# Kernel optimization log

Hardware: AMD Instinct MI355X
Metric: run time of the kernel (lower is better)

The kernel has to match this reference:

```python
import jax, jax.numpy as jnp
import numpy as np

N = 10000; E = 320000; B = 262144
F_NODE = 64; F_EDGE = 8; H = 4; C = 32
EVO_IN = C * 4 * H + 1      # 513
EVO_HID = 256; EVO_DIM = 64
FLOW_IN = EVO_DIM + 5       # 69
FLOW_HID = 256
SLOPE = 0.01                # torch LeakyReLU default slope
GAT_SLOPE = 0.2             # GATv2 attention LeakyReLU slope
EPS = 1e-5                  # BatchNorm eps


def setup_inputs() -> dict:
    key = jax.random.key(0)
    ks = iter(jax.random.split(key, 64))
    def nrm(shape, scale=1.0):
        return jax.random.normal(next(ks), shape, jnp.float32) * scale
    inp = {}
    inp['x1'] = nrm((N, F_NODE))
    inp['edge_index1'] = jax.random.randint(next(ks), (2, E), 0, N)
    inp['edge_attr1'] = nrm((E, F_EDGE))
    inp['x2'] = nrm((N, F_NODE))
    inp['edge_index2'] = jax.random.randint(next(ks), (2, E), 0, N)
    inp['edge_attr2'] = nrm((E, F_EDGE))
    inp['dist_m'] = jax.random.uniform(next(ks), (N, N), jnp.float32)
    inp['node_visit'] = jax.random.uniform(next(ks), (N, 2), jnp.float32)
    inp['od_nodes'] = jax.random.randint(next(ks), (B, 2), 0, N)
    # GATv2Conv params per snapshot: lin_l, lin_r (bias=True), lin_edge (bias=False), att [H,C], out bias [H*C]
    for p in ('g1', 'g2'):
        s = 1.0 / np.sqrt(F_NODE)
        inp[p + '_Wl'] = nrm((H * C, F_NODE), s)
        inp[p + '_bl'] = jnp.zeros((H * C,), jnp.float32)
        inp[p + '_Wr'] = nrm((H * C, F_NODE), s)
        inp[p + '_br'] = jnp.zeros((H * C,), jnp.float32)
        inp[p + '_We'] = nrm((H * C, F_EDGE), 1.0 / np.sqrt(F_EDGE))
        inp[p + '_att'] = nrm((H, C), 1.0 / np.sqrt(C))
        inp[p + '_bias'] = jnp.zeros((H * C,), jnp.float32)
    # EvoEmbedding (all Linear bias=False)
    inp['e_W1'] = nrm((EVO_HID, EVO_IN), 1.0 / np.sqrt(EVO_IN))
    inp['e_W2'] = nrm((EVO_HID, EVO_HID), 1.0 / np.sqrt(EVO_HID))
    inp['e_W3'] = nrm((EVO_HID, EVO_HID), 1.0 / np.sqrt(EVO_HID))
    inp['e_W4'] = nrm((EVO_HID // 2, EVO_HID), 1.0 / np.sqrt(EVO_HID))
    inp['e_Wout'] = nrm((EVO_DIM, EVO_HID // 2), 1.0 / np.sqrt(EVO_HID // 2))
    # FlowGenerator (Linear bias=False) + BatchNorm affine params
    inp['f_W1'] = nrm((FLOW_HID, FLOW_IN), 1.0 / np.sqrt(FLOW_IN))
    inp['f_W2'] = nrm((FLOW_HID, FLOW_HID), 1.0 / np.sqrt(FLOW_HID))
    inp['f_W3'] = nrm((FLOW_HID, FLOW_HID), 1.0 / np.sqrt(FLOW_HID))
    inp['f_W4'] = nrm((FLOW_HID // 2, FLOW_HID), 1.0 / np.sqrt(FLOW_HID))
    inp['f_Wout'] = nrm((1, FLOW_HID // 2), 1.0 / np.sqrt(FLOW_HID // 2))
    inp['f_g1'] = jnp.ones((FLOW_HID,), jnp.float32);  inp['f_b1'] = jnp.zeros((FLOW_HID,), jnp.float32)
    inp['f_g2'] = jnp.ones((FLOW_HID,), jnp.float32);  inp['f_b2'] = jnp.zeros((FLOW_HID,), jnp.float32)
    inp['f_g3'] = jnp.ones((FLOW_HID,), jnp.float32);  inp['f_b3'] = jnp.zeros((FLOW_HID,), jnp.float32)
    inp['f_g4'] = jnp.ones((FLOW_HID // 2,), jnp.float32); inp['f_b4'] = jnp.zeros((FLOW_HID // 2,), jnp.float32)
    return inp


def _gatv2(x, ei, ea, Wl, bl, Wr, br, We, att, bias):
    src, dst = ei[0], ei[1]
    # self-loops with fill_value='mean': per-target mean of incoming edge_attr
    deg = jax.ops.segment_sum(jnp.ones_like(dst, jnp.float32), dst, N)
    mean_attr = jax.ops.segment_sum(ea, dst, N) / jnp.maximum(deg, 1.0)[:, None]
    loops = jnp.arange(N)
    s = jnp.concatenate([src, loops]); d = jnp.concatenate([dst, loops])
    eaf = jnp.concatenate([ea, mean_attr], axis=0)            # [E+N, F_EDGE]
    xl = (x @ Wl.T + bl).reshape(N, H, C)                     # source transform
    xr = (x @ Wr.T + br).reshape(N, H, C)                     # target transform
    em = (eaf @ We.T).reshape(-1, H, C)
    msg = jax.nn.leaky_relu(xl[s] + xr[d] + em, GAT_SLOPE)    # [E+N, H, C]
    scr = jnp.einsum('ehc,hc->eh', msg, att)                  # [E+N, H]
    mx = jax.ops.segment_max(scr, d, N)
    ex = jnp.exp(scr - mx[d])
    den = jax.ops.segment_sum(ex, d, N)
    alpha = ex / den[d]                                       # softmax over incoming edges
    out = jax.ops.segment_sum(alpha[:, :, None] * xl[s], d, N).reshape(N, H * C) + bias
    return jax.nn.relu(out), alpha


def _evo(v, W1, W2, W3, W4, Wout):
    h = jax.nn.leaky_relu(v @ W1.T, SLOPE)
    h = jax.nn.leaky_relu(h @ W2.T, SLOPE)
    h = jax.nn.leaky_relu(h @ W3.T, SLOPE)
    h = jax.nn.leaky_relu(h @ W4.T, SLOPE)
    return h @ Wout.T


def _bn(x, g, b):
    mu = x.mean(0)
    var = x.var(0)
    return (x - mu) * jax.lax.rsqrt(var + EPS) * g + b


def _flow(v, W1, W2, W3, W4, Wout, g1, b1, g2, b2, g3, b3, g4, b4):
    h = jax.nn.leaky_relu(_bn(v @ W1.T, g1, b1), SLOPE)
    h = jax.nn.leaky_relu(_bn(h @ W2.T, g2, b2), SLOPE)
    h = jax.nn.leaky_relu(_bn(h @ W3.T, g3, b3), SLOPE)
    h = jax.nn.leaky_relu(_bn(h @ W4.T, g4, b4), SLOPE)
    return (h @ Wout.T).squeeze(-1)


def reference(x1, edge_index1, edge_attr1, x2, edge_index2, edge_attr2, dist_m, node_visit, od_nodes,
              g1_Wl, g1_bl, g1_Wr, g1_br, g1_We, g1_att, g1_bias,
              g2_Wl, g2_bl, g2_Wr, g2_br, g2_We, g2_att, g2_bias,
              e_W1, e_W2, e_W3, e_W4, e_Wout,
              f_W1, f_W2, f_W3, f_W4, f_Wout,
              f_g1, f_b1, f_g2, f_b2, f_g3, f_b3, f_g4, f_b4):
    n1, a1 = _gatv2(x1, edge_index1, edge_attr1, g1_Wl, g1_bl, g1_Wr, g1_br, g1_We, g1_att, g1_bias)
    n2, a2 = _gatv2(x2, edge_index2, edge_attr2, g2_Wl, g2_bl, g2_Wr, g2_br, g2_We, g2_att, g2_bias)
    o = od_nodes[:, 0]; dn = od_nodes[:, 1]
    dist = dist_m[o, dn][:, None]                              # fused gather replacing python loop
    feat = jnp.concatenate([n1[o], n1[dn], n2[o], n2[dn], dist], axis=1)  # [B, 513]
    evo = _evo(feat, e_W1, e_W2, e_W3, e_W4, e_Wout)           # [B, EVO_DIM]
    # NOTE: original uses node_visit[:,0] for BOTH o_visit and d_visit (kept faithful)
    ov = node_visit[o, 0:1]; dv = node_visit[dn, 0:1]
    ovn = node_visit[o, 1:2]; dvn = node_visit[dn, 1:2]
    cat = jnp.concatenate([evo, ov, dv, ovn, dvn, dist], axis=1)  # [B, 69]
    inferred = _flow(cat, f_W1, f_W2, f_W3, f_W4, f_Wout, f_g1, f_b1, f_g2, f_b2, f_g3, f_b3, f_g4, f_b4)
    return (inferred, a1, a2, evo)
```

## Files before the change

kernel.cpp:

```cpp
#include <hip/hip_runtime.h>

typedef unsigned short u16;
typedef unsigned int u32;

#define NN 10000
#define NE 320000
#define ET 330000
#define NB 262144
#define SHST 1792

typedef __attribute__((ext_vector_type(8))) short bf16x8;
typedef __attribute__((ext_vector_type(4))) float f32x4;

__device__ __forceinline__ u16 f2b(float f) {
  u32 u = __float_as_uint(f);
  u += 0x7fffu + ((u >> 16) & 1u);
  return (u16)(u >> 16);
}
__device__ __forceinline__ float b2f(u16 h) {
  return __uint_as_float(((u32)h) << 16);
}
__device__ __forceinline__ float lrelu(float v, float s) { return v > 0.f ? v : v * s; }

__device__ __forceinline__ void g2lds16(const void* g, void* l) {
  __builtin_amdgcn_global_load_lds((const __attribute__((address_space(1))) void*)g,
                                   (__attribute__((address_space(3))) void*)l, 16, 0, 0);
}

template <int N> __device__ __forceinline__ void waitv() {
  if constexpr (N == 0) asm volatile("s_waitcnt vmcnt(0)" ::: "memory");
  else if constexpr (N == 1) asm volatile("s_waitcnt vmcnt(1)" ::: "memory");
  else if constexpr (N == 2) asm volatile("s_waitcnt vmcnt(2)" ::: "memory");
  else if constexpr (N == 3) asm volatile("s_waitcnt vmcnt(3)" ::: "memory");
  else if constexpr (N == 4) asm volatile("s_waitcnt vmcnt(4)" ::: "memory");
  else if constexpr (N == 5) asm volatile("s_waitcnt vmcnt(5)" ::: "memory");
  else asm volatile("s_waitcnt vmcnt(6)" ::: "memory");
}
__device__ __forceinline__ void waitl0() { asm volatile("s_waitcnt lgkmcnt(0)" ::: "memory"); }
__device__ __forceinline__ void fence() { asm volatile("" ::: "memory"); }

__global__ __launch_bounds__(256) void k_prep(const float* __restrict__ eW2, const float* __restrict__ eW3,
                                              const float* __restrict__ eW4, const float* __restrict__ eWo,
                                              const float* __restrict__ fW1, const float* __restrict__ fW2,
                                              const float* __restrict__ fW3, const float* __restrict__ fW4,
                                              const float* __restrict__ eW1,
                                              u16* eW2b, u16* eW3b, u16* eW4b,
                                              u16* fW2b, u16* fW3b, u16* fW4b,
                                              float* W1T, float* w512, u16* wTail) {
  const int blk = blockIdx.x, tid = threadIdx.x;
  if (blk < 256) {
    int t = blk * 256 + tid; eW2b[t] = f2b(eW2[t]);
  } else if (blk < 512) {
    int t = (blk - 256) * 256 + tid; eW3b[t] = f2b(eW3[t]);
  } else if (blk < 640) {
    int t = (blk - 512) * 256 + tid; eW4b[t] = f2b(eW4[t]);
  } else if (blk < 896) {
    int t = (blk - 640) * 256 + tid; fW2b[t] = f2b(fW2[t]);
  } else if (blk < 1152) {
    int t = (blk - 896) * 256 + tid; fW3b[t] = f2b(fW3[t]);
  } else if (blk < 1280) {
    int t = (blk - 1152) * 256 + tid; fW4b[t] = f2b(fW4[t]);
  } else if (blk < 1536) {
    int m = blk - 1280;
    for (int k = tid; k < 512; k += 256) W1T[(size_t)k * 256 + m] = eW1[(size_t)m * 513 + k];
  } else if (blk == 1536) {
    w512[tid] = eW1[(size_t)tid * 513 + 512];
  } else if (blk < 1577) {
    int t = (blk - 1537) * 256 + tid;
    int r = t / 160, k = t - r * 160;
    wTail[(size_t)r * 160 + k] = (k < 128) ? f2b(eWo[(size_t)r * 128 + k]) : (u16)0;
  } else {
    int m = blk - 1577;
    int k = tid;
    if (k < 160) {
      float v = 0.f;
      if (k < 128) {
        const float* fr = fW1 + (size_t)m * 69;
        for (int j = 0; j < 64; ++j) v += fr[j] * eWo[(size_t)j * 128 + k];
      } else if (k < 133) {
        v = fW1[(size_t)m * 69 + 64 + (k - 128)];
      }
      wTail[(size_t)(64 + m) * 160 + k] = f2b(v);
    }
  }
}

__global__ __launch_bounds__(256) void k_sprep(const int* __restrict__ od, const float* __restrict__ dm,
                                               const float* __restrict__ nv,
                                               float* __restrict__ distb, u16* __restrict__ bufC) {
  int b = blockIdx.x * 256 + threadIdx.x;
  int o = od[b * 2], d = od[b * 2 + 1];
  float dist = dm[(size_t)o * NN + d];
  distb[b] = dist;
  u16 tmp[32];
  tmp[0] = f2b(nv[o * 2]);
  tmp[1] = f2b(nv[d * 2]);
  tmp[2] = f2b(nv[o * 2 + 1]);
  tmp[3] = f2b(nv[d * 2 + 1]);
  tmp[4] = f2b(dist);
#pragma unroll
  for (int k = 5; k < 32; ++k) tmp[k] = 0;
  u16* p = bufC + (size_t)b * 160 + 128;
#pragma unroll
  for (int k = 0; k < 4; ++k) *(bf16x8*)(p + k * 8) = *(bf16x8*)(tmp + k * 8);
}

__global__ __launch_bounds__(256) void k_count2(const int* __restrict__ ei0, const int* __restrict__ ei1,
                                                int* __restrict__ cnt) {
  int t = blockIdx.x * 256 + threadIdx.x;
  if (t >= 2 * ET) return;
  int g = t >= ET; int e = t - g * ET;
  const int* ei = g ? ei1 : ei0;
  int d = (e < NE) ? ei[NE + e] : (e - NE);
  atomicAdd(&cnt[g * NN + d], 1);
}

__global__ __launch_bounds__(1024) void k_scan2(const int* __restrict__ cnt, int* __restrict__ cs) {
  const int g = blockIdx.x;
  cnt += g * NN; cs += g * (NN + 1);
  __shared__ int part[1024];
  int tid = threadIdx.x;
  int base = tid * 10;
  int local[10];
  int s = 0;
#pragma unroll
  for (int i = 0; i < 10; ++i) {
    int idx = base + i;
    int v = (idx < NN) ? cnt[idx] : 0;
    local[i] = s; s += v;
  }
  part[tid] = s;
  __syncthreads();
  for (int off = 1; off < 1024; off <<= 1) {
    int v = (tid >= off) ? part[tid - off] : 0;
    __syncthreads();
    part[tid] += v;
    __syncthreads();
  }
  int pre = (tid > 0) ? part[tid - 1] : 0;
#pragma unroll
  for (int i = 0; i < 10; ++i) {
    int idx = base + i;
    if (idx < NN) cs[idx] = pre + local[i];
  }
  if (tid == 1023) cs[NN] = part[1023];
}

__global__ __launch_bounds__(256) void k_fill2(const int* __restrict__ ei0, const int* __restrict__ ei1,
                                               const int* __restrict__ cs, int* __restrict__ wr,
                                               int2* __restrict__ csr) {
  int t = blockIdx.x * 256 + threadIdx.x;
  if (t >= 2 * ET) return;
  int g = t >= ET; int e = t - g * ET;
  const int* ei = g ? ei1 : ei0;
  int s, d;
  if (e < NE) { s = ei[e]; d = ei[NE + e]; } else { s = e - NE; d = s; }
  int pos = atomicAdd(&wr[g * NN + d], 1);
// ... 158 lines not shown
  nout[(size_t)d * 128 + 64 + lane] = fmaxf(acc1 / dn1 + bias[64 + lane], 0.f);
}

__global__ __launch_bounds__(256) void k_alpha2(const float* __restrict__ scr,
                                                const int* __restrict__ ei0, const int* __restrict__ ei1,
                                                const float* __restrict__ m, const float* __restrict__ den,
                                                float* __restrict__ a1, float* __restrict__ a2) {
  int t = blockIdx.x * 256 + threadIdx.x;
  if (t >= 2 * ET * 4) return;
  int g = t >= ET * 4; int tt = t - g * ET * 4;
  int e = tt >> 2, h = tt & 3;
  const int* ei = g ? ei1 : ei0;
  int d = (e < NE) ? ei[NE + e] : (e - NE);
  const float* mg = m + (size_t)g * NN * 4;
  const float* dg = den + (size_t)g * NN * 4;
  float* aout = g ? a2 : a1;
  aout[tt] = __expf(scr[(size_t)g * ET * 4 + tt] - mg[d * 4 + h]) / dg[d * 4 + h];
}

__global__ __launch_bounds__(256) void k_qtab(const float* __restrict__ n1, const float* __restrict__ n2,
                                              const float* __restrict__ W1T,
                                              u16* __restrict__ Qo, u16* __restrict__ Qd) {
  __shared__ float s1[2048], s2[2048];
  int nb = blockIdx.x * 16;
  for (int i = threadIdx.x; i < 2048; i += 256) {
    s1[i] = n1[(size_t)nb * 128 + i];
    s2[i] = n2[(size_t)nb * 128 + i];
  }
  __syncthreads();
  int m = threadIdx.x;
  float qo[16], qd[16];
#pragma unroll
  for (int i = 0; i < 16; ++i) { qo[i] = 0.f; qd[i] = 0.f; }
#pragma unroll 2
  for (int k = 0; k < 128; ++k) {
    float w0 = W1T[(size_t)k * 256 + m];
    float w1 = W1T[(size_t)(128 + k) * 256 + m];
    float w2 = W1T[(size_t)(256 + k) * 256 + m];
    float w3 = W1T[(size_t)(384 + k) * 256 + m];
#pragma unroll
    for (int i = 0; i < 16; ++i) {
      float a = s1[i * 128 + k], b = s2[i * 128 + k];
      qo[i] += a * w0 + b * w2;
      qd[i] += a * w1 + b * w3;
    }
  }
#pragma unroll
  for (int i = 0; i < 16; ++i) {
    Qo[(size_t)(nb + i) * 256 + m] = f2b(qo[i]);
    Qd[(size_t)(nb + i) * 256 + m] = f2b(qd[i]);
  }
}

template <int NF, int EPI, int BNA>
__global__ __launch_bounds__(512) void gemm256(const u16* __restrict__ A, const u16* __restrict__ W,
                                               int K, size_t lda,
                                               u16* __restrict__ obf, int ld_bf,
                                               float* __restrict__ stats,
                                               const float* __restrict__ stin, const float* __restrict__ gg,
                                               const float* __restrict__ bb, float invB) {
  constexpr int M = NF * 64;
  constexpr int CPW = 2 + NF / 2;
  __shared__ alignas(16) u16 Alds[2][256 * 32];
  __shared__ alignas(16) u16 Blds[2][M * 32];
  __shared__ float sS[256], sT[256];
  const int tid = threadIdx.x;
  const int lane = tid & 63;
  const int w = tid >> 6;
  const int wr = w >> 2, wc = w & 3;
  const size_t rowBase = (size_t)blockIdx.x * 256;

  if (BNA) {
    for (int c = tid; c < K; c += 512) {
      float s0 = 0.f, q0 = 0.f;
#pragma unroll
      for (int sh = 0; sh < 8; ++sh) {
        s0 += stin[sh * SHST + c];
        q0 += stin[sh * SHST + K + c];
      }
      float mu = s0 * invB;
      float var = q0 * invB - mu * mu;
      float sc = rsqrtf(var + 1e-5f) * gg[c];
      sS[c] = sc;
      sT[c] = bb[c] - mu * sc;
    }
    __syncthreads();
  }

  f32x4 acc[8][NF];
  const f32x4 z4 = {0.f, 0.f, 0.f, 0.f};
#pragma unroll
  for (int m = 0; m < 8; ++m)
#pragma unroll
    for (int n = 0; n < NF; ++n) acc[m][n] = z4;

  const int crow = lane >> 2;
  const int ccol = (lane & 3) << 3;
  const int KT = K >> 5;

  auto stage = [&](int buf, int kb) {
#pragma unroll
    for (int i = 0; i < CPW; ++i) {
      const int c = w * CPW + i;
      if (c < 16) {
        const u16* src = A + (rowBase + (c << 4) + crow) * lda + kb + ccol;
        g2lds16(src, &Alds[buf][(c << 4) << 5]);
// ... 39 lines not shown
    for (int m = 0; m < 8; ++m) {
      bf16x8 af = *(const bf16x8*)&Alds[cur][(((wr << 7) + (m << 4) + lr) << 5) + lk];
      if (BNA) {
        bf16x8 o;
#pragma unroll
        for (int j = 0; j < 8; ++j) {
          float v = fmaf(b2f((u16)af[j]), sv[j], tv[j]);
          v = v > 0.f ? v : v * 0.01f;
          o[j] = (short)f2b(v);
        }
        af = o;
      }
#pragma unroll
      for (int n = 0; n < NF; ++n)
        acc[m][n] = __builtin_amdgcn_mfma_f32_16x16x32_bf16(af, bfr[n], acc[m][n], 0, 0, 0);
    }
    __builtin_amdgcn_s_barrier();
    cur ^= 1;
  }

  float csm[NF], cq[NF];
#pragma unroll
  for (int n = 0; n < NF; ++n) { csm[n] = 0.f; cq[n] = 0.f; }
#pragma unroll
  for (int m = 0; m < 8; ++m) {
#pragma unroll
    for (int n = 0; n < NF; ++n) {
      const int col = wc * (NF * 16) + (n << 4) + lr;
#pragma unroll
      for (int j = 0; j < 4; ++j) {
        const size_t row = rowBase + (wr << 7) + (m << 4) + (lg << 2) + j;
        float v = acc[m][n][j];
        if (EPI == 0) {
          v = v > 0.f ? v : v * 0.01f;
          obf[row * ld_bf + col] = f2b(v);
        } else {
          obf[row * ld_bf + col] = f2b(v);
          csm[n] += v; cq[n] += v * v;
        }
      }
    }
  }
  if (EPI == 1) {
    const int shard = ((int)blockIdx.x & 7) * SHST;
#pragma unroll
    for (int n = 0; n < NF; ++n) {
      float s = csm[n], q = cq[n];
      s += __shfl_xor(s, 16); s += __shfl_xor(s, 32);
      q += __shfl_xor(q, 16); q += __shfl_xor(q, 32);
      if (lane < 16) {
        const int col = wc * (NF * 16) + (n << 4) + lane;
        atomicAdd(&stats[shard + col], s);
        atomicAdd(&stats[shard + M + col], q);
      }
    }
  }
}

__global__ __launch_bounds__(512) void gemm256_evo(const u16* __restrict__ W,
                                                   u16* __restrict__ obf,
                                                   const u16* __restrict__ Qo, const u16* __restrict__ Qd,
                                                   const int* __restrict__ od, const float* __restrict__ distb,
                                                   const float* __restrict__ w512) {
  constexpr int KT = 8;
  __shared__ alignas(16) u16 Alds[2][256 * 32];
  __shared__ alignas(16) u16 Blds[2][256 * 32];
  __shared__ float sW[256], sDist[256];
  __shared__ int sO[256], sD[256];
  const int tid = threadIdx.x;
  const int lane = tid & 63;
  const int w = tid >> 6;
  const int wr = w >> 2, wc = w & 3;
  const size_t rowBase = (size_t)blockIdx.x * 256;
  const int crow = lane >> 2, ccol = (lane & 3) << 3;
  const int arow = tid >> 1;
  const int acol = (tid & 1) << 4;
  const int lr = lane & 15, lk = (lane >> 4) << 3, lg = lane >> 4;

  if (tid < 256) {
    int2 p = ((const int2*)od)[rowBase + tid];
    sO[tid] = p.x; sD[tid] = p.y;
    sDist[tid] = distb[rowBase + tid];
    sW[tid] = w512[tid];
  }
  __syncthreads();

  auto stageB = [&](int buf, int kb) {
#pragma unroll
    for (int i = 0; i < 2; ++i) {
      int c = w * 2 + i;
      const u16* src = W + (size_t)((c << 4) + crow) * 256 + kb + ccol;
      g2lds16(src, &Blds[buf][(c << 4) << 5]);
    }
  };
  auto loadA = [&](int kb, bf16x8& r0, bf16x8& r1, bf16x8& r2, bf16x8& r3) {
    const u16* qo = Qo + (size_t)sO[arow] * 256 + kb + acol;
    const u16* qd = Qd + (size_t)sD[arow] * 256 + kb + acol;
    r0 = *(const bf16x8*)qo; r1 = *(const bf16x8*)(qo + 8);
    r2 = *(const bf16x8*)qd; r3 = *(const bf16x8*)(qd + 8);
  };
  auto writeA = [&](int buf, int kb, bf16x8 r0, bf16x8 r1, bf16x8 r2, bf16x8 r3) {
    float dist = sDist[arow];
    bf16x8 w0, w1;
#pragma unroll
    for (int j = 0; j < 8; ++j) {
      float v = b2f((u16)r0[j]) + b2f((u16)r2[j]) + dist * sW[kb + acol + j];
      w0[j] = (short)f2b(lrelu(v, 0.01f));
      float v2 = b2f((u16)r1[j]) + b2f((u16)r3[j]) + dist * sW[kb + acol + 8 + j];
      w1[j] = (short)f2b(lrelu(v2, 0.01f));
    }
    *(bf16x8*)&Alds[buf][arow * 32 + acol] = w0;
    *(bf16x8*)&Alds[buf][arow * 32 + acol + 8] = w1;
  };

  f32x4 acc[8][4];
  const f32x4 z4 = {0.f, 0.f, 0.f, 0.f};
#pragma unroll
  for (int m = 0; m < 8; ++m)
#pragma unroll
    for (int n = 0; n < 4; ++n) acc[m][n] = z4;

  bf16x8 p0, p1, p2, p3;
  {
    bf16x8 c0, c1, c2, c3;
    loadA(0, c0, c1, c2, c3);
    writeA(0, 0, c0, c1, c2, c3);
  }
  stageB(0, 0);
  fence();
  loadA(32, p0, p1, p2, p3);
  fence();
  waitv<4>();
  waitl0();
  __builtin_amdgcn_s_barrier();

  int cur = 0;
  for (int kt = 0; kt < KT; ++kt) {
    const int kb = kt << 5;
    const bool hasN = kt + 1 < KT, hasNN = kt + 2 < KT;
    bf16x8 bfr[4];
#pragma unroll
    for (int n = 0; n < 4; ++n)
      bfr[n] = *(const bf16x8*)&Blds[cur][((((wc << 2) + n) << 4) + lr) * 32 + lk];
    if (hasN) stageB(cur ^ 1, kb + 32);
    fence();
    bf16x8 q0, q1, q2, q3;
    if (hasNN) loadA(kb + 64, q0, q1, q2, q3);
    fence();
#pragma unroll
    for (int m = 0; m < 8; ++m) {
      bf16x8 af = *(const bf16x8*)&Alds[cur][(((wr << 7) + (m << 4) + lr) << 5) + lk];
#pragma unroll
      for (int n = 0; n < 4; ++n)
        acc[m][n] = __builtin_amdgcn_mfma_f32_16x16x32_bf16(af, bfr[n], acc[m][n], 0, 0, 0);
    }
    if (hasN) {
      if (hasNN) waitv<6>(); else waitv<2>();
      writeA(cur ^ 1, kb + 32, p0, p1, p2, p3);
      p0 = q0; p1 = q1; p2 = q2; p3 = q3;
      if (hasNN) waitv<4>(); else waitv<0>();
      waitl0();
    }
    __builtin_amdgcn_s_barrier();
    cur ^= 1;
  }

#pragma unroll
  for (int m = 0; m < 8; ++m) {
#pragma unroll
    for (int n = 0; n < 4; ++n) {
      const int col = (wc << 6) + (n << 4) + lr;
#pragma unroll
      for (int j = 0; j < 4; ++j) {
        const size_t row = rowBase + (wr << 7) + (m << 4) + (lg << 2) + j;
        float v = acc[m][n][j];
        v = v > 0.f ? v : v * 0.01f;
        obf[row * 256 + col] = f2b(v);
      }
    }
  }
}

__global__ __launch_bounds__(512) void gemm320(const u16* __restrict__ A, const u16* __restrict__ W,
                                               float* __restrict__ oevo, u16* __restrict__ opre,
                                               float* __restrict__ stats) {
  constexpr int KT = 5;
  __shared__ alignas(16) u16 Alds[2][256 * 32];
  __shared__ alignas(16) u16 Blds[2][320 * 32];
  const int tid = threadIdx.x;
  const int lane = tid & 63;
  const int w = tid >> 6;
  const int wr = w >> 2, wc = w & 3;
  const size_t rowBase = (size_t)blockIdx.x * 256;
  const int crow = lane >> 2, ccol = (lane & 3) << 3;
  const int lr = lane & 15, lk = (lane >> 4) << 3, lg = lane >> 4;

  f32x4 acc[8][5];
  const f32x4 z4 = {0.f, 0.f, 0.f, 0.f};
#pragma unroll
  for (int m = 0; m < 8; ++m)
#pragma unroll
    for (int n = 0; n < 5; ++n) acc[m][n] = z4;

  auto stage = [&](int buf, int kb) {
#pragma unroll
    for (int i = 0; i < 2; ++i) {
      int c = w * 2 + i;
      const u16* src = A + (rowBase + (c << 4) + crow) * 160 + kb + ccol;
      g2lds16(src, &Alds[buf][(c << 4) << 5]);
    }
    if (w < 4) {
#pragma unroll
      for (int i = 0; i < 3; ++i) {
        int c = w * 3 + i;
        const u16* src = W + (size_t)((c << 4) + crow) * 160 + kb + ccol;
        g2lds16(src, &Blds[buf][(c << 4) << 5]);
      }
    } else {
#pragma unroll
      for (int i = 0; i < 2; ++i) {
        int c = 12 + (w - 4) * 2 + i;
        const u16* src = W + (size_t)((c << 4) + crow) * 160 + kb + ccol;
        g2lds16(src, &Blds[buf][(c << 4) << 5]);
      }
    }
  };

  stage(0, 0);
  int cur = 0;
  for (int kt = 0; kt < KT; ++kt) {
    if (kt + 1 < KT) {
      stage(cur ^ 1, (kt + 1) << 5);
      if (w < 4) waitv<5>(); else waitv<4>();
    } else {
      waitv<0>();
    }
    __builtin_amdgcn_s_barrier();
    bf16x8 bfr[5];
#pragma unroll
    for (int n = 0; n < 5; ++n)
      bfr[n] = *(const bf16x8*)&Blds[cur][(((wc * 80 + (n << 4) + lr)) << 5) + lk];
#pragma unroll
    for (int m = 0; m < 8; ++m) {
      bf16x8 af = *(const bf16x8*)&Alds[cur][(((wr << 7) + (m << 4) + lr) << 5) + lk];
#pragma unroll
      for (int n = 0; n < 5; ++n)
        acc[m][n] = __builtin_amdgcn_mfma_f32_16x16x32_bf16(af, bfr[n], acc[m][n], 0, 0, 0);
    }
    __builtin_amdgcn_s_barrier();
    cur ^= 1;
  }

  float csm[5], cq[5];
#pragma unroll
  for (int n = 0; n < 5; ++n) { csm[n] = 0.f; cq[n] = 0.f; }
#pragma unroll
  for (int m = 0; m < 8; ++m) {
#pragma unroll
    for (int n = 0; n < 5; ++n) {
      const int col = wc * 80 + (n << 4) + lr;
#pragma unroll
      for (int j = 0; j < 4; ++j) {
        const size_t row = rowBase + (wr << 7) + (m << 4) + (lg << 2) + j;
        float v = acc[m][n][j];
        if (col < 64) {
          oevo[row * 64 + col] = v;
        } else {
          opre[row * 256 + (col - 64)] = f2b(v);
          csm[n] += v; cq[n] += v * v;
        }
      }
    }
  }
  const int shard = ((int)blockIdx.x & 7) * SHST;
#pragma unroll
  for (int n = 0; n < 5; ++n) {
    float s = csm[n], q = cq[n];
    s += __shfl_xor(s, 16); s += __shfl_xor(s, 32);
    q += __shfl_xor(q, 16); q += __shfl_xor(q, 32);
    if (lane < 16) {
      const int col = wc * 80 + (n << 4) + lane;
      if (col >= 64) {
        atomicAdd(&stats[shard + col - 64], s);
        atomicAdd(&stats[shard + 256 + col - 64], q);
      }
    }
  }
}

__global__ __launch_bounds__(256) void k_fout4(const u16* __restrict__ pre, const float* __restrict__ st,
                                               const float* __restrict__ g, const float* __restrict__ b,
                                               const float* __restrict__ W, float* __restrict__ out,
                                               float invB) {
  __shared__ float smu[128], srs[128], sg[128], sb[128], sw[128];
  if (threadIdx.x < 128) {
    int c = threadIdx.x;
    float s0 = 0.f, q0 = 0.f;
#pragma unroll
    for (int sh = 0; sh < 8; ++sh) {
      s0 += st[sh * SHST + c];
      q0 += st[sh * SHST + 128 + c];
    }
    float mu = s0 * invB;
    float var = q0 * invB - mu * mu;
    smu[c] = mu;
    srs[c] = rsqrtf(var + 1e-5f);
    sg[c] = g[c];
    sb[c] = b[c];
    sw[c] = W[c];
  }
  __syncthreads();
  int bi = blockIdx.x * 256 + threadIdx.x;
  const u16* hp = pre + (size_t)bi * 128;
  float acc = 0.f;
#pragma unroll
  for (int k = 0; k < 128; k += 8) {
    bf16x8 u = *(const bf16x8*)(hp + k);
#pragma unroll
    for (int j = 0; j < 8; ++j) {
      int c = k + j;
      float v = (b2f((u16)u[j]) - smu[c]) * srs[c] * sg[c] + sb[c];
      v = b2f(f2b(lrelu(v, 0.01f)));
      acc += v * sw[c];
    }
  }
  out[bi] = acc;
}

extern "C" void kernel_launch(void* const* d_in, const int* in_sizes, int n_in,
                              void* d_out, int out_size, void* d_ws, size_t ws_size,
                              hipStream_t stream) {
  (void)in_sizes; (void)n_in; (void)out_size; (void)ws_size;

  const float* x0 = (const float*)d_in[0];
  const int* ei0 = (const int*)d_in[1];
  const float* ea0 = (const float*)d_in[2];
  const float* x1 = (const float*)d_in[3];
  const int* ei1 = (const int*)d_in[4];
  const float* ea1 = (const float*)d_in[5];
  const float* dm = (const float*)d_in[6];
  const float* nv = (const float*)d_in[7];
  const int* od = (const int*)d_in[8];
  const float* Wl0 = (const float*)d_in[9];
  const float* bl0 = (const float*)d_in[10];
  const float* Wr0 = (const float*)d_in[11];
  const float* br0 = (const float*)d_in[12];
  const float* We0 = (const float*)d_in[13];
  const float* att0 = (const float*)d_in[14];
  const float* bia0 = (const float*)d_in[15];
  const float* Wl1 = (const float*)d_in[16];
  const float* bl1 = (const float*)d_in[17];
  const float* Wr1 = (const float*)d_in[18];
  const float* br1 = (const float*)d_in[19];
  const float* We1 = (const float*)d_in[20];
  const float* att1 = (const float*)d_in[21];
  const float* bia1 = (const float*)d_in[22];
  const float* eW1 = (const float*)d_in[23];
  const float* eW2 = (const float*)d_in[24];
  const float* eW3 = (const float*)d_in[25];
  const float* eW4 = (const float*)d_in[26];
  const float* eWo = (const float*)d_in[27];
  const float* fW1 = (const float*)d_in[28];
  const float* fW2 = (const float*)d_in[29];
  const float* fW3 = (const float*)d_in[30];
  const float* fW4 = (const float*)d_in[31];
  const float* fWo = (const float*)d_in[32];
  const float* fg[4] = {(const float*)d_in[33], (const float*)d_in[35], (const float*)d_in[37], (const float*)d_in[39]};
  const float* fb[4] = {(const float*)d_in[34], (const float*)d_in[36], (const float*)d_in[38], (const float*)d_in[40]};

  float* out_inf = (float*)d_out;
  float* out_a1 = out_inf + NB;
  float* out_a2 = out_a1 + (size_t)ET * 4;
  float* out_evo = out_a2 + (size_t)ET * 4;

  char* base = (char*)d_ws;
  size_t cur = 0;
  auto carve = [&](size_t bytes) -> char* {
    char* p = base + cur;
    cur += (bytes + 255) & ~(size_t)255;
    return p;
  };
  u16* bufA = (u16*)carve((size_t)NB * 256 * 2);
  u16* bufB = (u16*)carve((size_t)NB * 256 * 2);
  u16* bufC = (u16*)carve((size_t)NB * 160 * 2);
  float* n1 = (float*)carve((size_t)NN * 128 * 4);
  float* n2 = (float*)carve((size_t)NN * 128 * 4);
  u16* Qob = (u16*)carve((size_t)NN * 256 * 2);
  u16* Qdb = (u16*)carve((size_t)NN * 256 * 2);
  float* xl = (float*)carve((size_t)2 * NN * 128 * 4);
  float* xr = (float*)carve((size_t)2 * NN * 128 * 4);
  float* stats = (float*)carve((size_t)8 * SHST * 4);
  int* cw = (int*)carve((size_t)4 * NN * 4);
  int* cnt = cw;
  int* wr = cw + 2 * NN;
  int* cs = (int*)carve((size_t)2 * (NN + 1) * 4);
  int2* csr = (int2*)carve((size_t)2 * ET * 8);
  float* m_out = (float*)carve((size_t)2 * NN * 4 * 4);
  float* den_out = (float*)carve((size_t)2 * NN * 4 * 4);
  float* asum = (float*)carve((size_t)2 * NN * 8 * 4);
  float* scr = (float*)carve((size_t)2 * ET * 4 * 4);
  float* distb = (float*)carve((size_t)NB * 4);
  float* w512 = (float*)carve(1024);
  float* W1T = (float*)carve(512 * 256 * 4);
  float* st[4] = {stats, stats + 512, stats + 1024, stats + 1536};
  u16* eW2b = (u16*)carve(256 * 256 * 2);
  u16* eW3b = (u16*)carve(256 * 256 * 2);
  u16* eW4b = (u16*)carve(128 * 256 * 2);
  u16* fW2b = (u16*)carve(256 * 256 * 2);
  u16* fW3b = (u16*)carve(256 * 256 * 2);
  u16* fW4b = (u16*)carve(128 * 256 * 2);
  u16* wTail = (u16*)carve(320 * 160 * 2);

  k_prep<<<1833, 256, 0, stream>>>(eW2, eW3, eW4, eWo, fW1, fW2, fW3, fW4, eW1,
                                   eW2b, eW3b, eW4b, fW2b, fW3b, fW4b,
                                   W1T, w512, wTail);
  hipMemsetAsync(stats, 0, (size_t)8 * SHST * 4 + (size_t)4 * NN * 4, stream);
  k_sprep<<<NB / 256, 256, 0, stream>>>(od, dm, nv, distb, bufC);

  k_count2<<<(2 * ET + 255) / 256, 256, 0, stream>>>(ei0, ei1, cnt);
  k_scan2<<<2, 1024, 0, stream>>>(cnt, cs);
  k_fill2<<<(2 * ET + 255) / 256, 256, 0, stream>>>(ei0, ei1, cs, wr, csr);
  k_asum2<<<2 * NN / 4, 256, 0, stream>>>(csr, cs, ea0, ea1, asum);
  k_xlr2<<<NN, 256, 0, stream>>>(x0, x1, Wl0, bl0, Wr0, br0, Wl1, bl1, Wr1, br1, xl, xr);
  k_scr2<<<4096, 256, 0, stream>>>(xl, xr, ei0, ei1, ea0, ea1, asum, We0, We1, att0, att1, scr);
  k_nodered2<<<2 * NN / 4, 256, 0, stream>>>(scr, csr, cs, xl, bia0, bia1, m_out, den_out, n1, n2);
  k_alpha2<<<(2 * ET * 4 + 255) / 256, 256, 0, stream>>>(scr, ei0, ei1, m_out, den_out, out_a1, out_a2);

  k_qtab<<<NN / 16, 256, 0, stream>>>(n1, n2, W1T, Qob, Qdb);

  const float invB = 1.0f / (float)NB;
  const int GB = NB / 256;
  gemm256_evo<<<GB, 512, 0, stream>>>(eW2b, bufA, Qob, Qdb, od, distb, w512);
  gemm256<4, 0, 0><<<GB, 512, 0, stream>>>(bufA, eW3b, 256, 256, bufB, 256, nullptr,
                                           nullptr, nullptr, nullptr, 0.f);
  gemm256<2, 0, 0><<<GB, 512, 0, stream>>>(bufB, eW4b, 256, 256, bufC, 160, nullptr,
                                           nullptr, nullptr, nullptr, 0.f);
  gemm320<<<GB, 512, 0, stream>>>(bufC, wTail, out_evo, bufA, st[0]);

  gemm256<4, 1, 1><<<GB, 512, 0, stream>>>(bufA, fW2b, 256, 256, bufB, 256, st[1],
                                           st[0], fg[0], fb[0], invB);
  gemm256<4, 1, 1><<<GB, 512, 0, stream>>>(bufB, fW3b, 256, 256, bufA, 256, st[2],
                                           st[1], fg[1], fb[1], invB);
  gemm256<2, 1, 1><<<GB, 512, 0, stream>>>(bufA, fW4b, 256, 256, bufB, 128, st[3],
                                           st[2], fg[2], fb[2], invB);
  k_fout4<<<NB / 256, 256, 0, stream>>>(bufB, st[3], fg[3], fb[3], fWo, out_inf, invB);
}
```

Before: 1.248 ms.

## Fuse four evo-embedding GEMMs into one kernel keeping activations in LDS

Result: slower. 1.798 ms (+44.0%).

```diff
diff --git a/kernel.cpp b/kernel.cpp
--- a/kernel.cpp
+++ b/kernel.cpp
@@ -38,6 +38,10 @@
 }
 __device__ __forceinline__ void waitl0() { asm volatile("s_waitcnt lgkmcnt(0)" ::: "memory"); }
 __device__ __forceinline__ void fence() { asm volatile("" ::: "memory"); }
+
+__device__ __forceinline__ int HIDX(int row, int col) {
+  return (row * 256 + col) ^ ((row & 7) << 3);
+}
 
 __global__ __launch_bounds__(256) void k_prep(const float* __restrict__ eW2, const float* __restrict__ eW3,
                                               const float* __restrict__ eW4, const float* __restrict__ eWo,
@@ -87,22 +91,19 @@
 
 __global__ __launch_bounds__(256) void k_sprep(const int* __restrict__ od, const float* __restrict__ dm,
                                                const float* __restrict__ nv,
-                                               float* __restrict__ distb, u16* __restrict__ bufC) {
+                                               float* __restrict__ distb, u16* __restrict__ sbuf) {
   int b = blockIdx.x * 256 + threadIdx.x;
   int o = od[b * 2], d = od[b * 2 + 1];
   float dist = dm[(size_t)o * NN + d];
   distb[b] = dist;
-  u16 tmp[32];
-  tmp[0] = f2b(nv[o * 2]);
-  tmp[1] = f2b(nv[d * 2]);
-  tmp[2] = f2b(nv[o * 2 + 1]);
-  tmp[3] = f2b(nv[d * 2 + 1]);
-  tmp[4] = f2b(dist);
-#pragma unroll
-  for (int k = 5; k < 32; ++k) tmp[k] = 0;
-  u16* p = bufC + (size_t)b * 160 + 128;
-#pragma unroll
-  for (int k = 0; k < 4; ++k) *(bf16x8*)(p + k * 8) = *(bf16x8*)(tmp + k * 8);
+  bf16x8 r;
+  r[0] = (short)f2b(nv[o * 2]);
+  r[1] = (short)f2b(nv[d * 2]);
+  r[2] = (short)f2b(nv[o * 2 + 1]);
+  r[3] = (short)f2b(nv[d * 2 + 1]);
+  r[4] = (short)f2b(dist);
+  r[5] = 0; r[6] = 0; r[7] = 0;
+  *(bf16x8*)(sbuf + (size_t)b * 8) = r;
 }
 
 __global__ __launch_bounds__(256) void k_count2(const int* __restrict__ ei0, const int* __restrict__ ei1,
@@ -367,6 +368,305 @@
   }
 }
 
+template <int NF2, int KK, int M2>
+__device__ __forceinline__ void fusedStage(const u16* __restrict__ Wsrc, u16* hT, u16* B2,
+                                           int tid, f32x4 acc[8][NF2]) {
+  const int lane = tid & 63, w = tid >> 6, wr = w >> 2, wc = w & 3;
+  const int lr = lane & 15, lk = (lane >> 4) << 3;
+  constexpr int KT = KK >> 5;
+  constexpr int NCH = (M2 * 4 + 511) / 512;
+  {
+    bf16x8 rB[NCH];
+    int c = 0;
+    for (int i = tid; i < M2 * 4; i += 512) {
+      int row = i >> 2, part = i & 3;
+      rB[c++] = *(const bf16x8*)(Wsrc + (size_t)row * KK + part * 8);
+    }
+    waitv<0>();
+    c = 0;
+    for (int i = tid; i < M2 * 4; i += 512) {
+      int row = i >> 2, part = i & 3;
+      *(bf16x8*)&B2[row * 40 + part * 8] = rB[c++];
+    }
+    waitl0();
+    __builtin_amdgcn_s_barrier();
+  }
+  for (int kt = 0; kt < KT; ++kt) {
+    const int kb = kt << 5;
+    bf16x8 af[8], bfr[NF2];
+#pragma unroll
+    for (int m = 0; m < 8; ++m) {
+      int row = (wr << 7) + (m << 4) + lr;
+      af[m] = *(const bf16x8*)&hT[HIDX(row, kb + lk)];
+    }
+#pragma unroll
+    for (int n = 0; n < NF2; ++n) {
+      int cc = wc * (NF2 * 16) + (n << 4) + lr;
+      bfr[n] = *(const bf16x8*)&B2[cc * 40 + lk];
+    }
+    bf16x8 rN[NCH];
+    if (kt + 1 < KT) {
+      int c = 0;
+      for (int i = tid; i < M2 * 4; i += 512) {
+        int row = i >> 2, part = i & 3;
+        rN[c++] = *(const bf16x8*)(Wsrc + (size_t)row * KK + kb + 32 + part * 8);
+      }
+    }
+#pragma unroll
+    for (int m = 0; m < 8; ++m)
+#pragma unroll
+      for (int n = 0; n < NF2; ++n)
+        acc[m][n] = __builtin_amdgcn_mfma_f32_16x16x32_bf16(af[m], bfr[n], acc[m][n], 0, 0, 0);
+    __builtin_amdgcn_s_barrier();
+    if (kt + 1 < KT) {
+      waitv<0>();
+      int c = 0;
+      for (int i = tid; i < M2 * 4; i += 512) {
+        int row = i >> 2, part = i & 3;
+        *(bf16x8*)&B2[row * 40 + part * 8] = rN[c++];
+      }
+      waitl0();
+    }
+    __builtin_amdgcn_s_barrier();
+  }
+}
+
+__global__ __launch_bounds__(512) void k_evochain(const u16* __restrict__ eW2b, const u16* __restrict__ eW3b,
+                                                  const u16* __restrict__ eW4b, const u16* __restrict__ wTail,
+                                                  const u16* __restrict__ Qo, const u16* __restrict__ Qd,
+                                                  const int* __restrict__ od, const float* __restrict__ distb,
+                                                  const float* __restrict__ w512, const u16* __restrict__ sbuf,
+                                                  float* __restrict__ oevo, u16* __restrict__ opre,
+                                                  float* __restrict__ stats) {
+  __shared__ alignas(16) u16 hT[65536];
+  __shared__ alignas(16) u16 B2[12800];
+  __shared__ alignas(16) float sAux[1024];
+  const int tid = threadIdx.x;
+  const int lane = tid & 63;
+  const int w = tid >> 6;
+  const int wr = w >> 2, wc = w & 3;
+  const size_t rowBase = (size_t)blockIdx.x * 256;
+  const int crow = lane >> 2, ccol = (lane & 3) << 3;
+  const int arow = tid >> 1, acol = (tid & 1) << 4;
+  const int lr = lane & 15, lk = (lane >> 4) << 3, lg = lane >> 4;
+
+  float* sW = sAux;
+  float* sDist = sAux + 256;
+  int* sO = (int*)(sAux + 512);
+  int* sD = (int*)(sAux + 768);
+
+  if (tid < 256) {
+    int2 p = ((const int2*)od)[rowBase + tid];
+    sO[tid] = p.x; sD[tid] = p.y;
+    sDist[tid] = distb[rowBase + tid];
+    sW[tid] = w512[tid];
+  }
+  __syncthreads();
+
+  {
+    u16* A0 = hT;
+    u16* B0 = hT + 16384;
+    auto stageB = [&](int buf, int kb) {
+#pragma unroll
+      for (int i = 0; i < 2; ++i) {
+        int c = w * 2 + i;
+        const u16* src = eW2b + (size_t)((c << 4) + crow) * 256 + kb + ccol;
+        g2lds16(src, B0 + buf * 8192 + (c << 9));
+      }
+    };
+    auto loadA = [&](int kb, bf16x8& r0, bf16x8& r1, bf16x8& r2, bf16x8& r3) {
+      const u16* qo = Qo + (size_t)sO[arow] * 256 + kb + acol;
+      const u16* qd = Qd + (size_t)sD[arow] * 256 + kb + acol;
+      r0 = *(const bf16x8*)qo; r1 = *(const bf16x8*)(qo + 8);
+      r2 = *(const bf16x8*)qd; r3 = *(const bf16x8*)(qd + 8);
+    };
+    auto writeA = [&](int buf, int kb, bf16x8 r0, bf16x8 r1, bf16x8 r2, bf16x8 r3) {
+      float dist = sDist[arow];
+      bf16x8 w0, w1;
+#pragma unroll
+      for (int j = 0; j < 8; ++j) {
+        float v = b2f((u16)r0[j]) + b2f((u16)r2[j]) + dist * sW[kb + acol + j];
+        w0[j] = (short)f2b(lrelu(v, 0.01f));
+        float v2 = b2f((u16)r1[j]) + b2f((u16)r3[j]) + dist * sW[kb + acol + 8 + j];
+        w1[j] = (short)f2b(lrelu(v2, 0.01f));
+      }
+      *(bf16x8*)(A0 + buf * 8192 + arow * 32 + acol) = w0;
+      *(bf16x8*)(A0 + buf * 8192 + arow * 32 + acol + 8) = w1;
+    };
+
+    f32x4 acc[8][4];
+    const f32x4 z4 = {0.f, 0.f, 0.f, 0.f};
+#pragma unroll
+    for (int m = 0; m < 8; ++m)
+#pragma unroll
+      for (int n = 0; n < 4; ++n) acc[m][n] = z4;
+
+    bf16x8 p0, p1, p2, p3;
+    {
+      bf16x8 c0, c1, c2, c3;
+      loadA(0, c0, c1, c2, c3);
+      writeA(0, 0, c0, c1, c2, c3);
+    }
+    stageB(0, 0);
+    fence();
+    loadA(32, p0, p1, p2, p3);
+    fence();
+    waitv<4>();
+    waitl0();
+    __builtin_amdgcn_s_barrier();
+
+    int cur = 0;
+    for (int kt = 0; kt < 8; ++kt) {
+      const int kb = kt << 5;
+      const bool hasN = kt + 1 < 8, hasNN = kt + 2 < 8;
+      bf16x8 bfr[4];
+#pragma unroll
+      for (int n = 0; n < 4; ++n)
+        bfr[n] = *(const bf16x8*)(B0 + cur * 8192 + ((((wc << 2) + n) << 4) + lr) * 32 + lk);
+      if (hasN) stageB(cur ^ 1, kb + 32);
+      fence();
+      bf16x8 q0, q1, q2, q3;
+      if (hasNN) loadA(kb + 64, q0, q1, q2, q3);
+      fence();
+#pragma unroll
+      for (int m = 0; m < 8; ++m) {
+        bf16x8 af = *(const bf16x8*)(A0 + cur * 8192 + (((wr << 7) + (m << 4) + lr) << 5) + lk);
+#pragma unroll
+        for (int n = 0; n < 4; ++n)
+          acc[m][n] = __builtin_amdgcn_mfma_f32_16x16x32_bf16(af, bfr[n], acc[m][n], 0, 0, 0);
+      }
+      if (hasN) {
+        if (hasNN) waitv<6>(); else waitv<2>();
+        writeA(cur ^ 1, kb + 32, p0, p1, p2, p3);
+        p0 = q0; p1 = q1; p2 = q2; p3 = q3;
+        if (hasNN) waitv<4>(); else waitv<0>();
+        waitl0();
+      }
+      __builtin_amdgcn_s_barrier();
+      cur ^= 1;
+    }
+#pragma unroll
+    for (int m = 0; m < 8; ++m)
+#pragma unroll
+      for (int n = 0; n < 4; ++n) {
+        const int col = (wc << 6) + (n << 4) + lr;
+#pragma unroll
+        for (int j = 0; j < 4; ++j) {
+          const int row = (wr << 7) + (m << 4) + (lg << 2) + j;
+          float v = acc[m][n][j];
+          v = v > 0.f ? v : v * 0.01f;
+          hT[HIDX(row, col)] = f2b(v);
+        }
+      }
+    waitl0();
+    __builtin_amdgcn_s_barrier();
+  }
+
+  {
+    f32x4 acc[8][4];
+    const f32x4 z4 = {0.f, 0.f, 0.f, 0.f};
+#pragma unroll
+    for (int m = 0; m < 8; ++m)
+#pragma unroll
+      for (int n = 0; n < 4; ++n) acc[m][n] = z4;
+    fusedStage<4, 256, 256>(eW3b, hT, B2, tid, acc);
+#pragma unroll
+    for (int m = 0; m < 8; ++m)
+#pragma unroll
+      for (int n = 0; n < 4; ++n) {
+        const int col = (wc << 6) + (n << 4) + lr;
+#pragma unroll
+        for (int j = 0; j < 4; ++j) {
+          const int row = (wr << 7) + (m << 4) + (lg << 2) + j;
+          float v = acc[m][n][j];
+          v = v > 0.f ? v : v * 0.01f;
+          hT[HIDX(row, col)] = f2b(v);
+        }
+      }
+    waitl0();
+    __builtin_amdgcn_s_barrier();
+  }
+
+  {
+    f32x4 acc[8][2];
+    const f32x4 z4 = {0.f, 0.f, 0.f, 0.f};
+#pragma unroll
+    for (int m = 0; m < 8; ++m)
+#pragma unroll
+      for (int n = 0; n < 2; ++n) acc[m][n] = z4;
+    fusedStage<2, 256, 128>(eW4b, hT, B2, tid, acc);
+#pragma unroll
+    for (int m = 0; m < 8; ++m)
+#pragma unroll
+      for (int n = 0; n < 2; ++n) {
+        const int col = (wc << 5) + (n << 4) + lr;
+#pragma unroll
+        for (int j = 0; j < 4; ++j) {
+          const int row = (wr << 7) + (m << 4) + (lg << 2) + j;
+          float v = acc[m][n][j];
+          v = v > 0.f ? v : v * 0.01f;
+          hT[HIDX(row, col)] = f2b(v);
+        }
+      }
+    if (tid < 256) {
+      bf16x8 s8 = *(const bf16x8*)(sbuf + (rowBase + tid) * 8);
+      *(bf16x8*)&hT[HIDX(tid, 128)] = s8;
+      bf16x8 z = {0, 0, 0, 0, 0, 0, 0, 0};
+      *(bf16x8*)&hT[HIDX(tid, 136)] = z;
+      *(bf16x8*)&hT[HIDX(tid, 144)] = z;
+      *(bf16x8*)&hT[HIDX(tid, 152)] = z;
+    }
+    waitl0();
+    __builtin_amdgcn_s_barrier();
+  }
+
+  {
+    f32x4 acc[8][5];
+    const f32x4 z4 = {0.f, 0.f, 0.f, 0.f};
+#pragma unroll
+    for (int m = 0; m < 8; ++m)
+#pragma unroll
+      for (int n = 0; n < 5; ++n) acc[m][n] = z4;
+    fusedStage<5, 160, 320>(wTail, hT, B2, tid, acc);
+
+    float csm[5], cq[5];
+#pragma unroll
+    for (int n = 0; n < 5; ++n) { csm[n] = 0.f; cq[n] = 0.f; }
+#pragma unroll
+    for (int m = 0; m < 8; ++m) {
+#pragma unroll
+      for (int n = 0; n < 5; ++n) {
+        const int col = wc * 80 + (n << 4) + lr;
+#pragma unroll
+        for (int j = 0; j < 4; ++j) {
+          const size_t row = rowBase + (wr << 7) + (m << 4) + (lg << 2) + j;
+          float v = acc[m][n][j];
+          if (col < 64) {
+            oevo[row * 64 + col] = v;
+          } else {
+            opre[row * 256 + (col - 64)] = f2b(v);
+            csm[n] += v; cq[n] += v * v;
+          }
+        }
+      }
+    }
+    const int shard = ((int)blockIdx.x & 7) * SHST;
+#pragma unroll
+    for (int n = 0; n < 5; ++n) {
+      float s = csm[n], q = cq[n];
+      s += __shfl_xor(s, 16); s += __shfl_xor(s, 32);
+      q += __shfl_xor(q, 16); q += __shfl_xor(q, 32);
+      if (lane < 16) {
+        const int col = wc * 80 + (n << 4) + lane;
+        if (col >= 64) {
+          atomicAdd(&stats[shard + col - 64], s);
+          atomicAdd(&stats[shard + 256 + col - 64], q);
+        }
+      }
+    }
+  }
+}
+
 template <int NF, int EPI, int BNA>
 __global__ __launch_bounds__(512) void gemm256(const u16* __restrict__ A, const u16* __restrict__ W,
                                                int K, size_t lda,
@@ -512,237 +812,6 @@
         const int col = wc * (NF * 16) + (n << 4) + lane;
         atomicAdd(&stats[shard + col], s);
         atomicAdd(&stats[shard + M + col], q);
-      }
-    }
-  }
-}
-
-__global__ __launch_bounds__(512) void gemm256_evo(const u16* __restrict__ W,
-                                                   u16* __restrict__ obf,
-                                                   const u16* __restrict__ Qo, const u16* __restrict__ Qd,
-                                                   const int* __restrict__ od, const float* __restrict__ distb,
-                                                   const float* __restrict__ w512) {
-  constexpr int KT = 8;
-  __shared__ alignas(16) u16 Alds[2][256 * 32];
-  __shared__ alignas(16) u16 Blds[2][256 * 32];
-  __shared__ float sW[256], sDist[256];
-  __shared__ int sO[256], sD[256];
-  const int tid = threadIdx.x;
-  const int lane = tid & 63;
-  const int w = tid >> 6;
-  const int wr = w >> 2, wc = w & 3;
-  const size_t rowBase = (size_t)blockIdx.x * 256;
-  const int crow = lane >> 2, ccol = (lane & 3) << 3;
-  const int arow = tid >> 1;
-  const int acol = (tid & 1) << 4;
-  const int lr = lane & 15, lk = (lane >> 4) << 3, lg = lane >> 4;
-
-  if (tid < 256) {
-    int2 p = ((const int2*)od)[rowBase + tid];
-    sO[tid] = p.x; sD[tid] = p.y;
-    sDist[tid] = distb[rowBase + tid];
-    sW[tid] = w512[tid];
-  }
-  __syncthreads();
-
-  auto stageB = [&](int buf, int kb) {
-#pragma unroll
-    for (int i = 0; i < 2; ++i) {
-      int c = w * 2 + i;
-      const u16* src = W + (size_t)((c << 4) + crow) * 256 + kb + ccol;
-      g2lds16(src, &Blds[buf][(c << 4) << 5]);
-    }
-  };
-  auto loadA = [&](int kb, bf16x8& r0, bf16x8& r1, bf16x8& r2, bf16x8& r3) {
-    const u16* qo = Qo + (size_t)sO[arow] * 256 + kb + acol;
-    const u16* qd = Qd + (size_t)sD[arow] * 256 + kb + acol;
-    r0 = *(const bf16x8*)qo; r1 = *(const bf16x8*)(qo + 8);
-    r2 = *(const bf16x8*)qd; r3 = *(const bf16x8*)(qd + 8);
-  };
-  auto writeA = [&](int buf, int kb, bf16x8 r0, bf16x8 r1, bf16x8 r2, bf16x8 r3) {
-    float dist = sDist[arow];
-    bf16x8 w0, w1;
-#pragma unroll
-    for (int j = 0; j < 8; ++j) {
-      float v = b2f((u16)r0[j]) + b2f((u16)r2[j]) + dist * sW[kb + acol + j];
-      w0[j] = (short)f2b(lrelu(v, 0.01f));
-      float v2 = b2f((u16)r1[j]) + b2f((u16)r3[j]) + dist * sW[kb + acol + 8 + j];
-      w1[j] = (short)f2b(lrelu(v2, 0.01f));
-    }
-    *(bf16x8*)&Alds[buf][arow * 32 + acol] = w0;
-    *(bf16x8*)&Alds[buf][arow * 32 + acol + 8] = w1;
-  };
-
-  f32x4 acc[8][4];
-  const f32x4 z4 = {0.f, 0.f, 0.f, 0.f};
-#pragma unroll
-  for (int m = 0; m < 8; ++m)
-#pragma unroll
-    for (int n = 0; n < 4; ++n) acc[m][n] = z4;
-
-  bf16x8 p0, p1, p2, p3;
-  {
-    bf16x8 c0, c1, c2, c3;
-    loadA(0, c0, c1, c2, c3);
-    writeA(0, 0, c0, c1, c2, c3);
-  }
-  stageB(0, 0);
-  fence();
-  loadA(32, p0, p1, p2, p3);
-  fence();
-  waitv<4>();
-  waitl0();
-  __builtin_amdgcn_s_barrier();
-
-  int cur = 0;
-  for (int kt = 0; kt < KT; ++kt) {
-    const int kb = kt << 5;
-    const bool hasN = kt + 1 < KT, hasNN = kt + 2 < KT;
-    bf16x8 bfr[4];
-#pragma unroll
-    for (int n = 0; n < 4; ++n)
-      bfr[n] = *(const bf16x8*)&Blds[cur][((((wc << 2) + n) << 4) + lr) * 32 + lk];
-    if (hasN) stageB(cur ^ 1, kb + 32);
-    fence();
-    bf16x8 q0, q1, q2, q3;
-    if (hasNN) loadA(kb + 64, q0, q1, q2, q3);
-    fence();
-#pragma unroll
-    for (int m = 0; m < 8; ++m) {
-      bf16x8 af = *(const bf16x8*)&Alds[cur][(((wr << 7) + (m << 4) + lr) << 5) + lk];
-#pragma unroll
-      for (int n = 0; n < 4; ++n)
-        acc[m][n] = __builtin_amdgcn_mfma_f32_16x16x32_bf16(af, bfr[n], acc[m][n], 0, 0, 0);
-    }
-    if (hasN) {
-      if (hasNN) waitv<6>(); else waitv<2>();
-      writeA(cur ^ 1, kb + 32, p0, p1, p2, p3);
-      p0 = q0; p1 = q1; p2 = q2; p3 = q3;
-      if (hasNN) waitv<4>(); else waitv<0>();
-      waitl0();
-    }
-    __builtin_amdgcn_s_barrier();
-    cur ^= 1;
-  }
-
-#pragma unroll
-  for (int m = 0; m < 8; ++m) {
-#pragma unroll
-    for (int n = 0; n < 4; ++n) {
-      const int col = (wc << 6) + (n << 4) + lr;
-#pragma unroll
-      for (int j = 0; j < 4; ++j) {
-        const size_t row = rowBase + (wr << 7) + (m << 4) + (lg << 2) + j;
-        float v = acc[m][n][j];
-        v = v > 0.f ? v : v * 0.01f;
-        obf[row * 256 + col] = f2b(v);
-      }
-    }
-  }
-}
-
-__global__ __launch_bounds__(512) void gemm320(const u16* __restrict__ A, const u16* __restrict__ W,
-                                               float* __restrict__ oevo, u16* __restrict__ opre,
-                                               float* __restrict__ stats) {
-  constexpr int KT = 5;
-  __shared__ alignas(16) u16 Alds[2][256 * 32];
-  __shared__ alignas(16) u16 Blds[2][320 * 32];
-  const int tid = threadIdx.x;
-  const int lane = tid & 63;
-  const int w = tid >> 6;
-  const int wr = w >> 2, wc = w & 3;
-  const size_t rowBase = (size_t)blockIdx.x * 256;
-  const int crow = lane >> 2, ccol = (lane & 3) << 3;
-  const int lr = lane & 15, lk = (lane >> 4) << 3, lg = lane >> 4;
-
-  f32x4 acc[8][5];
-  const f32x4 z4 = {0.f, 0.f, 0.f, 0.f};
-#pragma unroll
-  for (int m = 0; m < 8; ++m)
-#pragma unroll
-    for (int n = 0; n < 5; ++n) acc[m][n] = z4;
-
-  auto stage = [&](int buf, int kb) {
-#pragma unroll
-    for (int i = 0; i < 2; ++i) {
-      int c = w * 2 + i;
-      const u16* src = A + (rowBase + (c << 4) + crow) * 160 + kb + ccol;
-      g2lds16(src, &Alds[buf][(c << 4) << 5]);
-    }
-    if (w < 4) {
-#pragma unroll
-      for (int i = 0; i < 3; ++i) {
-        int c = w * 3 + i;
-        const u16* src = W + (size_t)((c << 4) + crow) * 160 + kb + ccol;
-        g2lds16(src, &Blds[buf][(c << 4) << 5]);
-      }
-    } else {
-#pragma unroll
-      for (int i = 0; i < 2; ++i) {
-        int c = 12 + (w - 4) * 2 + i;
-        const u16* src = W + (size_t)((c << 4) + crow) * 160 + kb + ccol;
-        g2lds16(src, &Blds[buf][(c << 4) << 5]);
-      }
-    }
-  };
-
-  stage(0, 0);
-  int cur = 0;
-  for (int kt = 0; kt < KT; ++kt) {
-    if (kt + 1 < KT) {
-      stage(cur ^ 1, (kt + 1) << 5);
-      if (w < 4) waitv<5>(); else waitv<4>();
-    } else {
-      waitv<0>();
-    }
-    __builtin_amdgcn_s_barrier();
-    bf16x8 bfr[5];
-#pragma unroll
-    for (int n = 0; n < 5; ++n)
-      bfr[n] = *(const bf16x8*)&Blds[cur][(((wc * 80 + (n << 4) + lr)) << 5) + lk];
-#pragma unroll
-    for (int m = 0; m < 8; ++m) {
-      bf16x8 af = *(const bf16x8*)&Alds[cur][(((wr << 7) + (m << 4) + lr) << 5) + lk];
-#pragma unroll
-      for (int n = 0; n < 5; ++n)
-        acc[m][n] = __builtin_amdgcn_mfma_f32_16x16x32_bf16(af, bfr[n], acc[m][n], 0, 0, 0);
-    }
-    __builtin_amdgcn_s_barrier();
-    cur ^= 1;
-  }
-
-  float csm[5], cq[5];
-#pragma unroll
-  for (int n = 0; n < 5; ++n) { csm[n] = 0.f; cq[n] = 0.f; }
-#pragma unroll
-  for (int m = 0; m < 8; ++m) {
-#pragma unroll
-    for (int n = 0; n < 5; ++n) {
-      const int col = wc * 80 + (n << 4) + lr;
-#pragma unroll
-      for (int j = 0; j < 4; ++j) {
-        const size_t row = rowBase + (wr << 7) + (m << 4) + (lg << 2) + j;
-        float v = acc[m][n][j];
-        if (col < 64) {
-          oevo[row * 64 + col] = v;
-        } else {
-          opre[row * 256 + (col - 64)] = f2b(v);
-          csm[n] += v; cq[n] += v * v;
-        }
-      }
-    }
-  }
-  const int shard = ((int)blockIdx.x & 7) * SHST;
-#pragma unroll
-  for (int n = 0; n < 5; ++n) {
-    float s = csm[n], q = cq[n];
-    s += __shfl_xor(s, 16); s += __shfl_xor(s, 32);
-    q += __shfl_xor(q, 16); q += __shfl_xor(q, 32);
-    if (lane < 16) {
-      const int col = wc * 80 + (n << 4) + lane;
-      if (col >= 64) {
-        atomicAdd(&stats[shard + col - 64], s);
-        atomicAdd(&stats[shard + 256 + col - 64], q);
       }
     }
   }
@@ -842,7 +911,7 @@
   };
   u16* bufA = (u16*)carve((size_t)NB * 256 * 2);
   u16* bufB = (u16*)carve((size_t)NB * 256 * 2);
-  u16* bufC = (u16*)carve((size_t)NB * 160 * 2);
+  u16* sbuf = (u16*)carve((size_t)NB * 8 * 2);
   float* n1 = (float*)carve((size_t)NN * 128 * 4);
   float* n2 = (float*)carve((size_t)NN * 128 * 4);
   u16* Qob = (u16*)carve((size_t)NN * 256 * 2);
@@ -875,7 +944,7 @@
                                    eW2b, eW3b, eW4b, fW2b, fW3b, fW4b,
                                    W1T, w512, wTail);
   hipMemsetAsync(stats, 0, (size_t)8 * SHST * 4 + (size_t)4 * NN * 4, stream);
-  k_sprep<<<NB / 256, 256, 0, stream>>>(od, dm, nv, distb, bufC);
+  k_sprep<<<NB / 256, 256, 0, stream>>>(od, dm, nv, distb, sbuf);
 
   k_count2<<<(2 * ET + 255) / 256, 256, 0, stream>>>(ei0, ei1, cnt);
   k_scan2<<<2, 1024, 0, stream>>>(cnt, cs);
@@ -890,12 +959,8 @@
 
   const float invB = 1.0f / (float)NB;
   const int GB = NB / 256;
-  gemm256_evo<<<GB, 512, 0, stream>>>(eW2b, bufA, Qob, Qdb, od, distb, w512);
-  gemm256<4, 0, 0><<<GB, 512, 0, stream>>>(bufA, eW3b, 256, 256, bufB, 256, nullptr,
-                                           nullptr, nullptr, nullptr, 0.f);
-  gemm256<2, 0, 0><<<GB, 512, 0, stream>>>(bufB, eW4b, 256, 256, bufC, 160, nullptr,
-                                           nullptr, nullptr, nullptr, 0.f);
-  gemm320<<<GB, 512, 0, stream>>>(bufC, wTail, out_evo, bufA, st[0]);
+  k_evochain<<<GB, 512, 0, stream>>>(eW2b, eW3b, eW4b, wTail, Qob, Qdb, od, distb, w512, sbuf,
+                                     out_evo, bufA, st[0]);
 
   gemm256<4, 1, 1><<<GB, 512, 0, stream>>>(bufA, fW2b, 256, 256, bufB, 256, st[1],
                                            st[0], fg[0], fb[0], invB);
```
